# Performance work log

Hardware: AMD Instinct MI355X
Metric: run time of the kernel (lower is better)

Reference implementation:

```python
import jax, jax.numpy as jnp
import numpy as np

B, C, H, W = 16, 512, 16, 64
T = 128
V, E, EH, DH = 600, 80, 256, 512


def _lstm_scan(x_seq, h0, c0, Wih, Whh, b):
    # x_seq: [S, N, in]; PyTorch gate order i,f,g,o
    def step(carry, x):
        h, c = carry
        g = x @ Wih.T + h @ Whh.T + b
        i, f, gg, o = jnp.split(g, 4, axis=-1)
        c_new = jax.nn.sigmoid(f) * c + jax.nn.sigmoid(i) * jnp.tanh(gg)
        h_new = jax.nn.sigmoid(o) * jnp.tanh(c_new)
        return (h_new, c_new), h_new
    (hT, cT), hs = jax.lax.scan(step, (h0, c0), x_seq)
    return hs, hT, cT


def setup_inputs():
    key = jax.random.key(0)
    ks = jax.random.split(key, 32)
    INIT = 0.01
    def u(k, shape, s):
        return jax.random.uniform(k, shape, jnp.float32, -s, s)
    se = 1.0 / np.sqrt(EH)
    sd = 1.0 / np.sqrt(DH)
    sc = 1.0 / np.sqrt(DH + 2 * EH)
    so = 1.0 / np.sqrt(EH)
    sv = 1.0 / np.sqrt(2 * EH)
    return {
        'features': jax.random.normal(ks[0], (B, C, H, W), jnp.float32),
        'formulas': jax.random.randint(ks[1], (B, T), 0, V),
        'Wih_f': u(ks[2], (4 * EH, C), se), 'Whh_f': u(ks[3], (4 * EH, EH), se),
        'bih_f': u(ks[4], (4 * EH,), se), 'bhh_f': u(ks[5], (4 * EH,), se),
        'Wih_b': u(ks[6], (4 * EH, C), se), 'Whh_b': u(ks[7], (4 * EH, EH), se),
        'bih_b': u(ks[8], (4 * EH,), se), 'bhh_b': u(ks[9], (4 * EH,), se),
        'emb': jax.random.normal(ks[10], (V, E), jnp.float32),
        'Wc_w': u(ks[11], (EH, DH + 2 * EH), sc), 'Wc_b': u(ks[12], (EH,), sc),
        'Wout_w': u(ks[13], (V, EH), so), 'Wout_b': u(ks[14], (V,), so),
        'Vh0': u(ks[15], (2, EH), INIT), 'Vc0': u(ks[16], (2, EH), INIT),
        'beta': u(ks[17], (DH,), INIT),
        'Wh_w': u(ks[18], (DH, DH), sd), 'Wh_b': u(ks[19], (DH,), sd),
        'Wv_w': u(ks[20], (DH, 2 * EH), sv), 'Wv_b': u(ks[21], (DH,), sv),
        'Wdec_ih': u(ks[22], (4 * DH, EH + E), sd), 'Wdec_hh': u(ks[23], (4 * DH, DH), sd),
        'bdec_ih': u(ks[24], (4 * DH,), sd), 'bdec_hh': u(ks[25], (4 * DH,), sd),
    }


def _forward(features, formulas, Wih_f, Whh_f, bih_f, bhh_f, Wih_b, Whh_b, bih_b, bhh_b,
             emb, Wc_w, Wc_b, Wout_w, Wout_b, Vh0, Vc0, beta, Wh_w, Wh_b, Wv_w, Wv_b,
             Wdec_ih, Wdec_hh, bdec_ih, bdec_hh):
    Bv, Cv, Hv, Wd = features.shape
    eh = Vh0.shape[1]
    # ---- row encoder: bidirectional LSTM over width, batch = B*H ----
    x = features.transpose(0, 2, 3, 1).reshape(Bv * Hv, Wd, Cv).transpose(1, 0, 2)  # [W, B*H, C]
    h0f = jnp.broadcast_to(Vh0[0], (Bv * Hv, eh)); c0f = jnp.broadcast_to(Vc0[0], (Bv * Hv, eh))
    h0b = jnp.broadcast_to(Vh0[1], (Bv * Hv, eh)); c0b = jnp.broadcast_to(Vc0[1], (Bv * Hv, eh))
    hs_f, hTf, cTf = _lstm_scan(x, h0f, c0f, Wih_f, Whh_f, bih_f + bhh_f)
    hs_b, hTb, cTb = _lstm_scan(x[::-1], h0b, c0b, Wih_b, Whh_b, bih_b + bhh_b)
    hs_b = hs_b[::-1]
    enc_out = jnp.concatenate([hs_f, hs_b], -1).transpose(1, 0, 2).reshape(Bv, Hv, Wd, 2 * eh)

    def convert(s):  # [2, B*H, eh] -> [B, 2*eh]: permute, merge directions, mean over H
        return s.reshape(2, Bv, Hv, eh).transpose(1, 2, 0, 3).reshape(Bv, Hv, 2 * eh).mean(axis=1)
    h0 = convert(jnp.stack([hTf, hTb]))
    c0 = convert(jnp.stack([cTf, cTb]))
    ctx0 = enc_out.mean(axis=(1, 2))
    O0 = jnp.tanh(jnp.concatenate([h0, ctx0], 1) @ Wc_w.T + Wc_b)

    Wv_enc = enc_out @ Wv_w.T + Wv_b  # hoisted: W_v(enc_out) is constant across decode steps

    def dec_step(carry, tgt):
        h, c, O = carry
        prev_y = emb[tgt]                                   # [B, E]
        inp = jnp.concatenate([prev_y, O], 1)
        g = inp @ Wdec_ih.T + h @ Wdec_hh.T + bdec_ih + bdec_hh
        i, f, gg, o = jnp.split(g, 4, axis=-1)
        c_t = jax.nn.sigmoid(f) * c + jax.nn.sigmoid(i) * jnp.tanh(gg)
        h_t = jax.nn.sigmoid(o) * jnp.tanh(c_t)
        lin_h = h @ Wh_w.T + Wh_b                           # NB: attention uses PREVIOUS h, as in source
        e = jnp.sum(beta * jnp.tanh(lin_h[:, None, None, :] + Wv_enc), -1)  # [B, H, W]
        alpha = jax.nn.softmax(e.reshape(Bv, -1), -1).reshape(Bv, Hv, Wd)
        context = jnp.einsum('bhw,bhwd->bd', alpha, enc_out)
        O_t = jnp.tanh(jnp.concatenate([h_t, context], 1) @ Wc_w.T + Wc_b)
        logit = jax.nn.softmax(O_t @ Wout_w.T + Wout_b, -1)  # eval-mode softmax
        return (h_t, c_t, O_t), logit

    _, logits = jax.lax.scan(dec_step, (h0, c0, O0), formulas.T)
    return logits.transpose(1, 0, 2)  # [B, T, V]


def reference(features, formulas, Wih_f, Whh_f, bih_f, bhh_f, Wih_b, Whh_b, bih_b, bhh_b,
              emb, Wc_w, Wc_b, Wout_w, Wout_b, Vh0, Vc0, beta, Wh_w, Wh_b, Wv_w, Wv_b,
              Wdec_ih, Wdec_hh, bdec_ih, bdec_hh):
    logits = _forward(features, formulas, Wih_f, Whh_f, bih_f, bhh_f, Wih_b, Whh_b, bih_b, bhh_b,
                      emb, Wc_w, Wc_b, Wout_w, Wout_b, Vh0, Vc0, beta, Wh_w, Wh_b, Wv_w, Wv_b,
                      Wdec_ih, Wdec_hh, bdec_ih, bdec_hh)
    targets = jnp.argmax(logits, axis=2)  # argmax(log(p)) == argmax(p)
    return logits, targets
```

## Files before the change

### kernel.cpp

```cpp
#include <hip/hip_runtime.h>
#include <math.h>

#define NB 16
#define NC 512
#define NH 16
#define NW 64
#define NT 128
#define NV 600
#define NE 80
#define EH 256
#define DH 512
#define NSEQ 256
#define GEH 1024
#define GDH 2048

typedef float f32x4 __attribute__((ext_vector_type(4)));

#define OFF_XPRE_F 0ull
#define OFF_XPRE_B 16777216ull
#define OFF_XT     33554432ull
#define OFF_ENC    41943040ull
#define OFF_WENC   50331648ull
#define OFF_WDT    50855936ull
#define OFF_WHT    52592640ull
#define OFF_WCT    52854784ull
#define OFF_WOUTT  53116928ull
#define OFF_HA     53270528ull
#define OFF_CENC   53532672ull
#define OFF_CDEC   53663744ull
#define OFF_CTX0   53671936ull
#define OFF_OKT    53680128ull
#define WS_FLOATS  53708800ull

__device__ __forceinline__ float sigf(float x) {
  return __builtin_amdgcn_rcpf(1.f + __expf(-x));
}
__device__ __forceinline__ float tanhfast(float x) {
  float e = __expf(2.f * x);
  return 1.f - 2.f * __builtin_amdgcn_rcpf(e + 1.f);
}

__global__ void k_transpose(float* __restrict__ dst, const float* __restrict__ src,
                            int R, int Cc) {
  int idx = blockIdx.x * 256 + threadIdx.x;
  if (idx >= R * Cc) return;
  int c = idx / R, r = idx - c * R;
  dst[idx] = src[(size_t)r * Cc + c];
}

__global__ void k_prep_wenc(float* __restrict__ dst, const float* __restrict__ whh, int dir) {
  int idx = blockIdx.x * 256 + threadIdx.x;
  int g = idx & 3, j = (idx >> 2) & 255, k = idx >> 10;
  dst[(size_t)dir * 262144 + idx] = whh[((size_t)(g * 256 + j)) * 256 + k];
}

__global__ void k_buildXt(float* __restrict__ Xt, const float* __restrict__ feat) {
  __shared__ float tile[64][65];
  int n = blockIdx.x, cb = blockIdx.y * 64;
  int b = n >> 4, hh = n & 15;
  int tid = threadIdx.x;
  for (int i = 0; i < 16; ++i) {
    int c = (tid >> 6) + i * 4;
    int w = tid & 63;
    tile[c][w] = feat[(((size_t)b * NC + cb + c) * NH + hh) * NW + w];
  }
  __syncthreads();
  for (int i = 0; i < 16; ++i) {
    int w = (tid >> 6) + i * 4;
    int ci = tid & 63;
    Xt[((size_t)(w * NSEQ + n)) * NC + cb + ci] = tile[ci][w];
  }
}

__global__ __launch_bounds__(256) void k_gemm_nt(
    const float* __restrict__ A, const float* __restrict__ Wt,
    const float* __restrict__ bias1, const float* __restrict__ bias2,
    float* __restrict__ Cout, int M, int Nn, int K) {
  __shared__ float As[128 * 32];
  __shared__ float Bs[128 * 32];
  int tid = threadIdx.x;
  int mb = blockIdx.x * 128, nb = blockIdx.y * 128;
  int tx = tid & 15, ty = tid >> 4;
  int row0 = ty * 8, col0 = tx * 8;
  float acc[8][8];
#pragma unroll
  for (int i = 0; i < 8; ++i)
#pragma unroll
    for (int j = 0; j < 8; ++j) acc[i][j] = 0.f;
  int lm = tid >> 1, lk = (tid & 1) * 8;
  int sw = 4 * ((lm >> 3) & 7);
  int p0 = (lk + sw) & 31, p1 = (lk + 4 + sw) & 31;
  const float* Ap = A + (size_t)(mb + lm) * K + lk;
  const float* Bp = Wt + (size_t)(nb + lm) * K + lk;
  for (int k0 = 0; k0 < K; k0 += 16) {
    float4 a0 = *(const float4*)(Ap + k0);
    float4 a1 = *(const float4*)(Ap + k0 + 4);
    float4 b0 = *(const float4*)(Bp + k0);
    float4 b1 = *(const float4*)(Bp + k0 + 4);
    __syncthreads();
    *(float4*)&As[lm * 32 + p0] = a0;
    *(float4*)&As[lm * 32 + p1] = a1;
    *(float4*)&Bs[lm * 32 + p0] = b0;
    *(float4*)&Bs[lm * 32 + p1] = b1;
    __syncthreads();
#pragma unroll
    for (int kq = 0; kq < 4; ++kq) {
      float4 av[8], bv[8];
#pragma unroll
      for (int i = 0; i < 8; ++i) {
        int m = row0 + i;
        av[i] = *(float4*)&As[m * 32 + ((kq * 4 + 4 * ((m >> 3) & 7)) & 31)];
      }
#pragma unroll
      for (int j = 0; j < 8; ++j) {
        int n = col0 + j;
        bv[j] = *(float4*)&Bs[n * 32 + ((kq * 4 + 4 * ((n >> 3) & 7)) & 31)];
      }
#pragma unroll
      for (int i = 0; i < 8; ++i)
#pragma unroll
        for (int j = 0; j < 8; ++j)
          acc[i][j] += av[i].x * bv[j].x + av[i].y * bv[j].y
                     + av[i].z * bv[j].z + av[i].w * bv[j].w;
    }
  }
  float bs[8];
#pragma unroll
  for (int j = 0; j < 8; ++j) {
    float v = bias1 ? bias1[nb + col0 + j] : 0.f;
    if (bias2) v += bias2[nb + col0 + j];
    bs[j] = v;
  }
  for (int i = 0; i < 8; ++i) {
    float* cp = Cout + (size_t)(mb + row0 + i) * Nn + nb + col0;
#pragma unroll
    for (int j = 0; j < 8; ++j) cp[j] = acc[i][j] + bs[j];
  }
}

__global__ __launch_bounds__(1024) void k_encoder_s(
    const float* __restrict__ wenc, const float* __restrict__ xpreF,
    const float* __restrict__ xpreB, const float* __restrict__ Vh0,
    const float* __restrict__ Vc0, float* __restrict__ encout,
    float* __restrict__ hT_out, float* __restrict__ cT_out) {
  __shared__ float hs[4][256];
  __shared__ float pacc[3][16][256];
  int bid = blockIdx.x;
  int dir = bid >> 6;
  int s0 = (bid & 63) * 4;
  int tid = threadIdx.x;
  int j = tid & 255, kq = tid >> 8;
  float c[4];
  if (kq == 0) {
    float h0 = Vh0[dir * 256 + j];
    float c0v = Vc0[dir * 256 + j];
#pragma unroll
    for (int s = 0; s < 4; ++s) { hs[s][j] = h0; c[s] = c0v; }
  }
  __syncthreads();
  const float* wp = wenc + (size_t)dir * 262144 + (size_t)(kq * 64) * 1024 + (size_t)j * 4;
  const float* xbase = dir ? xpreB : xpreF;
  for (int t = 0; t < 64; ++t) {
    int w = dir ? (63 - t) : t;
    float acc[4][4];
#pragma unroll
    for (int s = 0; s < 4; ++s)
#pragma unroll
      for (int g = 0; g < 4; ++g) acc[s][g] = 0.f;
#pragma unroll 8
    for (int k = 0; k < 64; ++k) {
      float4 w4 = *(const float4*)(wp + (size_t)k * 1024);
      int kk = kq * 64 + k;
      float h0k = hs[0][kk], h1k = hs[1][kk], h2k = hs[2][kk], h3k = hs[3][kk];
      acc[0][0] += w4.x * h0k; acc[0][1] += w4.y * h0k; acc[0][2] += w4.z * h0k; acc[0][3] += w4.w * h0k;
      acc[1][0] += w4.x * h1k; acc[1][1] += w4.y * h1k; acc[1][2] += w4.z * h1k; acc[1][3] += w4.w * h1k;
      acc[2][0] += w4.x * h2k; acc[2][1] += w4.y * h2k; acc[2][2] += w4.z * h2k; acc[2][3] += w4.w * h2k;
      acc[3][0] += w4.x * h3k; acc[3][1] += w4.y * h3k; acc[3][2] += w4.z * h3k; acc[3][3] += w4.w * h3k;
    }
    if (kq > 0) {
#pragma unroll
      for (int s = 0; s < 4; ++s)
#pragma unroll
        for (int g = 0; g < 4; ++g)
          pacc[kq - 1][s * 4 + g][j] = acc[s][g];
    }
    __syncthreads();
    if (kq == 0) {
#pragma unroll
      for (int s = 0; s < 4; ++s) {
        int n = s0 + s;
        const float* xp = xbase + ((size_t)w * NSEQ + n) * GEH;
        float g4[4];
#pragma unroll
        for (int g = 0; g < 4; ++g)
          g4[g] = acc[s][g] + pacc[0][s * 4 + g][j] + pacc[1][s * 4 + g][j]
                + pacc[2][s * 4 + g][j] + xp[g * 256 + j];
        float cn = sigf(g4[1]) * c[s] + sigf(g4[0]) * tanhfast(g4[2]);
        c[s] = cn;
        float hn = sigf(g4[3]) * tanhfast(cn);
        hs[s][j] = hn;
        encout[((size_t)n * NW + w) * (2 * EH) + dir * EH + j] = hn;
      }
    }
    __syncthreads();
  }
  if (kq == 0) {
#pragma unroll
    for (int s = 0; s < 4; ++s) {
      int n = s0 + s;
      hT_out[((size_t)(dir * NSEQ + n)) * EH + j] = hs[s][j];
      cT_out[((size_t)(dir * NSEQ + n)) * EH + j] = c[s];
    }
  }
}

__global__ void k_conv(const float* __restrict__ hA, const float* __restrict__ cE,
                       const float* __restrict__ enc, float* __restrict__ cdec,
                       float* __restrict__ okT, float* __restrict__ ctx0) {
  int b = blockIdx.x, tid = threadIdx.x;
  for (int d = tid; d < 512; d += 256) {
    float s = 0.f;
    for (int p = 0; p < 1024; ++p) s += enc[((size_t)b * 1024 + p) * 512 + d];
    ctx0[(size_t)b * 512 + d] = s * (1.f / 1024.f);
    int dir = d >> 8, u = d & 255;
    float sh = 0.f, sc_ = 0.f;
    for (int hh = 0; hh < 16; ++hh) {
      size_t idx = ((size_t)(dir * NSEQ + b * 16 + hh)) * EH + u;
      sh += hA[idx]; sc_ += cE[idx];
    }
    cdec[(size_t)b * 512 + d] = sc_ * (1.f / 16.f);
    okT[(size_t)(256 + d) * 16 + b] = sh * (1.f / 16.f);
  }
}

__global__ void k_O0v2(const float* __restrict__ okT, const float* __restrict__ ctx0,
                       const float* __restrict__ wcT, const float* __restrict__ wcb,
                       const float* __restrict__ whT, const float* __restrict__ whb,
                       float* __restrict__ okT_o, float* __restrict__ linh) {
  int b = blockIdx.x, tid = threadIdx.x;
  float a = wcb[tid];
  for (int k = 0; k < 512; ++k)
    a += okT[(size_t)(256 + k) * 16 + b] * wcT[(size_t)k * 256 + tid];
  const float* cb = ctx0 + (size_t)b * 512;
  for (int k = 0; k < 512; ++k)
    a += cb[k] * wcT[(size_t)(512 + k) * 256 + tid];
  okT_o[(size_t)tid * 16 + b] = tanhfast(a);
  for (int d = tid; d < 512; d += 256) {
    float v = whb[d];
    for (int k = 0; k < 512; ++k)
      v += okT[(size_t)(256 + k) * 16 + b] * whT[(size_t)k * 512 + d];
    linh[(size_t)b * 512 + d] = v;
  }
}

__global__ void k_embproj(const int* __restrict__ formulas, const float* __restrict__ emb,
                          const float* __restrict__ wdT, const float* __restrict__ b1,
                          const float* __restrict__ b2, float* __restrict__ ep) {
  int g = blockIdx.x * 256 + threadIdx.x;
  int tb = blockIdx.y;
  int b = tb & 15, t = tb >> 4;
  int tok = formulas[b * NT + t];
  const float* ev = emb + (size_t)tok * NE;
  float a = b1[g] + b2[g];
  for (int k = 0; k < NE; ++k) a += ev[k] * wdT[(size_t)k * GDH + g];
  ep[(size_t)tb * GDH + g] = a;
}

__device__ __forceinline__ void logits_block(
    int vc, int lane, int wq, const float* __restrict__ okT,
    const float* __restrict__ woutT, const float* __restrict__ woutb,
    float* __restrict__ ev, float* __restrict__ evp) {
  int v = vc * 64 + lane;
  bool valid = v < NV;
  int vl = valid ? v : (NV - 1);
  float acc[4] = {0.f, 0.f, 0.f, 0.f};
  for (int k = 0; k < 256; ++k) {
    float w = woutT[(size_t)k * NV + vl];
    float4 o4 = *(const float4*)&okT[(size_t)k * 16 + wq * 4];
    acc[0] += w * o4.x; acc[1] += w * o4.y; acc[2] += w * o4.z; acc[3] += w * o4.w;
  }
  float bs = woutb[vl];
#pragma unroll
  for (int i = 0; i < 4; ++i) {
    float e = valid ? __expf(acc[i] + bs) : 0.f;
    if (valid) ev[(size_t)(wq * 4 + i) * NV + v] = e;
    float s = e;
#pragma unroll
    for (int m = 1; m < 64; m <<= 1) s += __shfl_xor(s, m, 64);
    if (lane == 0) evp[(wq * 4 + i) * 16 + vc] = s;
  }
}

__device__ __forceinline__ void norm_block(
    int b, int tid, const float* __restrict__ ev, const float* __restrict__ evp,
    float* __restrict__ outp, int t) {
  float tot = 0.f;
#pragma unroll
  for (int i = 0; i < 10; ++i) tot += evp[b * 16 + i];
  float r = __builtin_amdgcn_rcpf(tot);
  float* orow = outp + ((size_t)b * NT + t) * NV;
  orow[tid] = ev[b * NV + tid] * r;
  orow[tid + 256] = ev[b * NV + tid + 256] * r;
  if (tid < 88) orow[tid + 512] = ev[b * NV + tid + 512] * r;
}

__global__ __launch_bounds__(256) void k_dec1(
    const float* __restrict__ okT, const float* __restrict__ wdT,
    const float* __restrict__ woutT, const float* __restrict__ woutb,
    const float* __restrict__ linh, const float* __restrict__ beta,
    const float* __restrict__ wvenc, const float* __restrict__ enc,
    float* __restrict__ gpart, float* __restrict__ ctxp,
    float* __restrict__ spart, float* __restrict__ ev, float* __restrict__ evp,
    int t) {
  __shared__ float sscore[32];
  __shared__ float cpart[4][512];
  int bid = blockIdx.x, tid = threadIdx.x;
  int lane = tid & 63, wq = tid >> 6;

  if (bid < 512) {
    int b = bid >> 5, pc2 = bid & 31;
    int d0 = lane * 8;
    float lh[8], bt[8];
    const float* lp = linh + (size_t)b * 512 + d0;
#pragma unroll
    for (int jj = 0; jj < 8; ++jj) { lh[jj] = lp[jj]; bt[jj] = beta[d0 + jj]; }
    float c8[8] = {0.f, 0.f, 0.f, 0.f, 0.f, 0.f, 0.f, 0.f};
#pragma unroll
    for (int pi = 0; pi < 8; ++pi) {
      int p = pc2 * 32 + wq * 8 + pi;
      const float* wvp = wvenc + ((size_t)(b * 1024 + p)) * 512 + d0;
      const float* erp = enc + ((size_t)(b * 1024 + p)) * 512 + d0;
      f32x4 wv0 = __builtin_nontemporal_load((const f32x4*)wvp);
      f32x4 wv1 = __builtin_nontemporal_load((const f32x4*)(wvp + 4));
      f32x4 e0 = __builtin_nontemporal_load((const f32x4*)erp);
      f32x4 e1 = __builtin_nontemporal_load((const f32x4*)(erp + 4));
      float e = bt[0] * tanhfast(lh[0] + wv0.x) + bt[1] * tanhfast(lh[1] + wv0.y)
              + bt[2] * tanhfast(lh[2] + wv0.z) + bt[3] * tanhfast(lh[3] + wv0.w)
              + bt[4] * tanhfast(lh[4] + wv1.x) + bt[5] * tanhfast(lh[5] + wv1.y)
              + bt[6] * tanhfast(lh[6] + wv1.z) + bt[7] * tanhfast(lh[7] + wv1.w);
#pragma unroll
      for (int m = 1; m < 64; m <<= 1) e += __shfl_xor(e, m, 64);
      float s = __expf(e);
      if (lane == 0) sscore[wq * 8 + pi] = s;
      c8[0] += s * e0.x; c8[1] += s * e0.y; c8[2] += s * e0.z; c8[3] += s * e0.w;
      c8[4] += s * e1.x; c8[5] += s * e1.y; c8[6] += s * e1.z; c8[7] += s * e1.w;
    }
#pragma unroll
    for (int jj = 0; jj < 8; ++jj) cpart[wq][d0 + jj] = c8[jj];
    __syncthreads();
    {
      int d = tid * 2;
      float r0 = cpart[0][d] + cpart[1][d] + cpart[2][d] + cpart[3][d];
      float r1 = cpart[0][d + 1] + cpart[1][d + 1] + cpart[2][d + 1] + cpart[3][d + 1];
      *(float2*)&ctxp[((size_t)(b * 32 + pc2)) * 512 + d] = make_float2(r0, r1);
    }
    if (tid == 0) {
      float s = 0.f;
#pragma unroll
      for (int p = 0; p < 32; ++p) s += sscore[p];
      spart[b * 32 + pc2] = s;
    }
  } else if (bid < 560) {
    int idx = bid - 512;
    int oc = idx / 6, kc = idx - oc * 6;
    int o = oc * 256 + tid, k0 = kc * 128;
    const float* wp = wdT + (size_t)(80 + k0) * GDH + o;
    const float* sp = okT + (size_t)k0 * 16;
    float acc[16];
#pragma unroll
    for (int i = 0; i < 16; ++i) acc[i] = 0.f;
    for (int kk = 0; kk < 128; ++kk) {
      float w = wp[(size_t)kk * GDH];
#pragma unroll
      for (int bb = 0; bb < 16; ++bb) acc[bb] += sp[kk * 16 + bb] * w;
    }
#pragma unroll
    for (int bb = 0; bb < 16; ++bb)
      gpart[((size_t)(kc * 16 + bb)) * GDH + o] = acc[bb];
  } else {
    if (t > 0) logits_block(bid - 560, lane, wq, okT, woutT, woutb, ev, evp);
  }
}

__global__ __launch_bounds__(256) void k_dec2(
    const float* __restrict__ gpart, const float* __restrict__ ep,
    const float* __restrict__ ctxp, const float* __restrict__ spart,
    const float* __restrict__ wcT, const float* __restrict__ wcb,
    const float* __restrict__ whT, const float* __restrict__ whb,
    const float* __restrict__ ev, const float* __restrict__ evp,
    float* __restrict__ cdecA, float* __restrict__ cdecB,
    float* __restrict__ okT, float* __restrict__ linh,
    float* __restrict__ outp, int t) {
  __shared__ float smem[1280];
  int bid = blockIdx.x, tid = threadIdx.x;
  if (bid < 64) {
    int b = bid >> 2, q = bid & 3;
    const float* cold = (t & 1) ? cdecB : cdecA;
    float* cnew = (t & 1) ? cdecA : cdecB;
    float Ssum = 0.f;
#pragma unroll
    for (int pc = 0; pc < 32; ++pc) Ssum += spart[b * 32 + pc];
    float rS = __builtin_amdgcn_rcpf(Ssum);
    {
      int d = tid * 2;
      float s0 = 0.f, s1 = 0.f;
#pragma unroll 4
      for (int pc = 0; pc < 32; ++pc) {
        float2 c2 = *(const float2*)&ctxp[((size_t)(b * 32 + pc)) * 512 + d];
        s0 += c2.x; s1 += c2.y;
      }
      smem[512 + d] = s0 * rS;
      smem[512 + d + 1] = s1 * rS;
    }
#pragma unroll
    for (int half = 0; half < 2; ++half) {
      int j = half * 256 + tid;
      float g4[4];
#pragma unroll
      for (int gi = 0; gi < 4; ++gi) {
        float v = ep[((size_t)(t * 16 + b)) * GDH + gi * 512 + j];
#pragma unroll
        for (int kc = 0; kc < 6; ++kc)
          v += gpart[((size_t)(kc * 16 + b)) * GDH + gi * 512 + j];
        g4[gi] = v;
      }
      size_t ci = (size_t)b * 512 + j;
      float cn = sigf(g4[1]) * cold[ci] + sigf(g4[0]) * tanhfast(g4[2]);
      cnew[ci] = cn;
      float hn = sigf(g4[3]) * tanhfast(cn);
      smem[j] = hn;
      okT[(size_t)(256 + j) * 16 + b] = hn;
    }
    __syncthreads();
    {
      int ol = tid & 63, kq = tid >> 6;
      int o = q * 64 + ol;
      float a = 0.f;
      const float* wp = wcT + (size_t)(kq * 256) * 256 + o;
      const float* sp = smem + kq * 256;
      for (int k = 0; k < 256; ++k) a += wp[(size_t)k * 256] * sp[k];
      smem[1024 + kq * 64 + ol] = a;
    }
    __syncthreads();
    if (tid < 64) {
      float s = smem[1024 + tid] + smem[1088 + tid] + smem[1152 + tid] + smem[1216 + tid];
      int o = q * 64 + tid;
      okT[(size_t)o * 16 + b] = tanhfast(s + wcb[o]);
    }
    __syncthreads();
    {
      int o2 = tid & 127, kh = tid >> 7;
      int o = q * 128 + o2;
      float a = 0.f;
      const float* wp = whT + (size_t)(kh * 256) * 512 + o;
      const float* sp = smem + kh * 256;
      for (int k = 0; k < 256; ++k) a += wp[(size_t)k * 512] * sp[k];
      smem[1024 + kh * 128 + o2] = a;
    }
    __syncthreads();
    if (tid < 128) {
      int o = q * 128 + tid;
      float s = smem[1024 + tid] + smem[1152 + tid];
      linh[(size_t)b * 512 + o] = s + whb[o];
    }
  } else {
    if (t > 0) norm_block(bid - 64, tid, ev, evp, outp, t - 1);
  }
}

__global__ __launch_bounds__(256) void k_log_tail(
    const float* __restrict__ okT, const float* __restrict__ woutT,
    const float* __restrict__ woutb, float* __restrict__ ev, float* __restrict__ evp) {
  int lane = threadIdx.x & 63, wq = threadIdx.x >> 6;
  logits_block(blockIdx.x, lane, wq, okT, woutT, woutb, ev, evp);
}

__global__ void k_norm(const float* __restrict__ ev, const float* __restrict__ evp,
                       float* __restrict__ outp, int t) {
  norm_block(blockIdx.x, threadIdx.x, ev, evp, outp, t);
}

__global__ void k_argmax(const float* __restrict__ outp, float* __restrict__ tgt) {
  int bt = blockIdx.x;
  int lane = threadIdx.x;
  const float* row = outp + (size_t)bt * NV;
  float bv = -1.f;
  int bi = 0;
  for (int v = lane; v < NV; v += 64) {
    float x = row[v];
    if (x > bv) { bv = x; bi = v; }
  }
#pragma unroll
  for (int m = 1; m < 64; m <<= 1) {
    float ov = __shfl_xor(bv, m, 64);
    int oi = __shfl_xor(bi, m, 64);
    if (ov > bv || (ov == bv && oi < bi)) { bv = ov; bi = oi; }
  }
  if (lane == 0) tgt[bt] = (float)bi;
}

extern "C" void kernel_launch(void* const* d_in, const int* in_sizes, int n_in,
                              void* d_out, int out_size, void* d_ws, size_t ws_size,
                              hipStream_t stream) {
  (void)in_sizes; (void)n_in; (void)out_size;
  if (ws_size < WS_FLOATS * sizeof(float)) return;

  const float* feat     = (const float*)d_in[0];
  const int*   formulas = (const int*)d_in[1];
  const float* Wih_f    = (const float*)d_in[2];
  const float* Whh_f    = (const float*)d_in[3];
  const float* bih_f    = (const float*)d_in[4];
  const float* bhh_f    = (const float*)d_in[5];
  const float* Wih_b    = (const float*)d_in[6];
  const float* Whh_b    = (const float*)d_in[7];
  const float* bih_b    = (const float*)d_in[8];
  const float* bhh_b    = (const float*)d_in[9];
  const float* emb      = (const float*)d_in[10];
  const float* Wc_w     = (const float*)d_in[11];
  const float* Wc_b     = (const float*)d_in[12];
  const float* Wout_w   = (const float*)d_in[13];
  const float* Wout_b   = (const float*)d_in[14];
  const float* Vh0      = (const float*)d_in[15];
  const float* Vc0      = (const float*)d_in[16];
  const float* beta     = (const float*)d_in[17];
  const float* Wh_w     = (const float*)d_in[18];
  const float* Wh_b     = (const float*)d_in[19];
  const float* Wv_w     = (const float*)d_in[20];
  const float* Wv_b     = (const float*)d_in[21];
  const float* Wdec_ih  = (const float*)d_in[22];
  const float* Wdec_hh  = (const float*)d_in[23];
  const float* bdec_ih  = (const float*)d_in[24];
  const float* bdec_hh  = (const float*)d_in[25];

  float* ws = (float*)d_ws;
  float* xpreF  = ws + OFF_XPRE_F;
  float* xpreB  = ws + OFF_XPRE_B;
  float* xt     = ws + OFF_XT;
  float* encout = ws + OFF_ENC;
  float* wenc   = ws + OFF_WENC;
  float* wdT    = ws + OFF_WDT;
  float* whT    = ws + OFF_WHT;
  float* wcT    = ws + OFF_WCT;
  float* woutT  = ws + OFF_WOUTT;
  float* hA     = ws + OFF_HA;
  float* cenc   = ws + OFF_CENC;
  float* cdecA  = ws + OFF_CDEC;
  float* ctx0   = ws + OFF_CTX0;
  float* okT    = ws + OFF_OKT;
  float* gpart  = xpreB;
  float* ctxp   = gpart + 196608;
  float* spart  = ctxp + 262144;
  float* ev     = spart + 512;
  float* evp    = ev + 9600;
  float* linh   = evp + 256;
  float* cdecB  = linh + 8192;
  float* embproj = xpreF;
  float* wvenc   = xt;

  float* out_logits = (float*)d_out;
  float* out_tgt    = out_logits + (size_t)NB * NT * NV;

  k_transpose<<<(2048 * 336 + 255) / 256, 256, 0, stream>>>(wdT, Wdec_ih, 2048, 336);
  k_transpose<<<(2048 * 512 + 255) / 256, 256, 0, stream>>>(wdT + 336 * 2048, Wdec_hh, 2048, 512);
  k_transpose<<<(512 * 512 + 255) / 256, 256, 0, stream>>>(whT, Wh_w, 512, 512);
  k_transpose<<<(256 * 1024 + 255) / 256, 256, 0, stream>>>(wcT, Wc_w, 256, 1024);
  k_transpose<<<(600 * 256 + 255) / 256, 256, 0, stream>>>(woutT, Wout_w, 600, 256);
  k_prep_wenc<<<1024, 256, 0, stream>>>(wenc, Whh_f, 0);
  k_prep_wenc<<<1024, 256, 0, stream>>>(wenc, Whh_b, 1);
  k_buildXt<<<dim3(256, 8), 256, 0, stream>>>(xt, feat);
  k_gemm_nt<<<dim3(128, 8), 256, 0, stream>>>(xt, Wih_f, bih_f, bhh_f, xpreF, 16384, 1024, 512);
  k_gemm_nt<<<dim3(128, 8), 256, 0, stream>>>(xt, Wih_b, bih_b, bhh_b, xpreB, 16384, 1024, 512);

  k_encoder_s<<<128, 1024, 0, stream>>>(wenc, xpreF, xpreB, Vh0, Vc0, encout, hA, cenc);

  k_gemm_nt<<<dim3(128, 4), 256, 0, stream>>>(encout, Wv_w, Wv_b, nullptr, wvenc, 16384, 512, 512);
  k_conv<<<16, 256, 0, stream>>>(hA, cenc, encout, cdecA, okT, ctx0);
  k_O0v2<<<16, 256, 0, stream>>>(okT, ctx0, wcT, Wc_b, whT, Wh_b, okT, linh);
  k_embproj<<<dim3(8, 2048), 256, 0, stream>>>(formulas, emb, wdT, bdec_ih, bdec_hh, embproj);

  for (int t = 0; t < NT; ++t) {
    k_dec1<<<570, 256, 0, stream>>>(okT, wdT, woutT, Wout_b, linh, beta, wvenc, encout,
                                    gpart, ctxp, spart, ev, evp, t);
    k_dec2<<<80, 256, 0, stream>>>(gpart, embproj, ctxp, spart, wcT, Wc_b, whT, Wh_b,
                                   ev, evp, cdecA, cdecB, okT, linh, out_logits, t);
  }
  k_log_tail<<<10, 256, 0, stream>>>(okT, woutT, Wout_b, ev, evp);
  k_norm<<<16, 256, 0, stream>>>(ev, evp, out_logits, NT - 1);
  k_argmax<<<NB * NT, 64, 0, stream>>>(out_logits, out_tgt);
}
```

Baseline: 7.547 ms.

## Split decoder attention over more blocks and tile embedding projection over tokens

```diff
diff --git a/kernel.cpp b/kernel.cpp
--- a/kernel.cpp
+++ b/kernel.cpp
@@ -253,17 +253,34 @@
   }
 }
 
-__global__ void k_embproj(const int* __restrict__ formulas, const float* __restrict__ emb,
-                          const float* __restrict__ wdT, const float* __restrict__ b1,
-                          const float* __restrict__ b2, float* __restrict__ ep) {
-  int g = blockIdx.x * 256 + threadIdx.x;
-  int tb = blockIdx.y;
-  int b = tb & 15, t = tb >> 4;
-  int tok = formulas[b * NT + t];
-  const float* ev = emb + (size_t)tok * NE;
-  float a = b1[g] + b2[g];
-  for (int k = 0; k < NE; ++k) a += ev[k] * wdT[(size_t)k * GDH + g];
-  ep[(size_t)tb * GDH + g] = a;
+__global__ __launch_bounds__(256) void k_embproj(
+    const int* __restrict__ formulas, const float* __restrict__ emb,
+    const float* __restrict__ wdT, const float* __restrict__ b1,
+    const float* __restrict__ b2, float* __restrict__ ep) {
+  __shared__ float se[32][NE];
+  int gc = blockIdx.x, tc = blockIdx.y;
+  int tid = threadIdx.x;
+  int g = gc * 256 + tid;
+  for (int i = tid; i < 32 * NE; i += 256) {
+    int ti = i / NE, k = i - ti * NE;
+    int tb = tc * 32 + ti;
+    int b = tb & 15, t = tb >> 4;
+    int tok = formulas[b * NT + t];
+    se[ti][k] = emb[(size_t)tok * NE + k];
+  }
+  __syncthreads();
+  float acc[32];
+  float bias = b1[g] + b2[g];
+#pragma unroll
+  for (int i = 0; i < 32; ++i) acc[i] = bias;
+  for (int k = 0; k < NE; ++k) {
+    float w = wdT[(size_t)k * GDH + g];
+#pragma unroll
+    for (int i = 0; i < 32; ++i) acc[i] += se[i][k] * w;
+  }
+#pragma unroll
+  for (int i = 0; i < 32; ++i)
+    ep[(size_t)(tc * 32 + i) * GDH + g] = acc[i];
 }
 
 __device__ __forceinline__ void logits_block(
@@ -312,13 +329,13 @@
     float* __restrict__ gpart, float* __restrict__ ctxp,
     float* __restrict__ spart, float* __restrict__ ev, float* __restrict__ evp,
     int t) {
-  __shared__ float sscore[32];
+  __shared__ float sscore[16];
   __shared__ float cpart[4][512];
   int bid = blockIdx.x, tid = threadIdx.x;
   int lane = tid & 63, wq = tid >> 6;
 
-  if (bid < 512) {
-    int b = bid >> 5, pc2 = bid & 31;
+  if (bid < 1024) {
+    int b = bid >> 6, pc = bid & 63;
     int d0 = lane * 8;
     float lh[8], bt[8];
     const float* lp = linh + (size_t)b * 512 + d0;
@@ -326,8 +343,8 @@
     for (int jj = 0; jj < 8; ++jj) { lh[jj] = lp[jj]; bt[jj] = beta[d0 + jj]; }
     float c8[8] = {0.f, 0.f, 0.f, 0.f, 0.f, 0.f, 0.f, 0.f};
 #pragma unroll
-    for (int pi = 0; pi < 8; ++pi) {
-      int p = pc2 * 32 + wq * 8 + pi;
+    for (int pi = 0; pi < 4; ++pi) {
+      int p = pc * 16 + wq * 4 + pi;
       const float* wvp = wvenc + ((size_t)(b * 1024 + p)) * 512 + d0;
       const float* erp = enc + ((size_t)(b * 1024 + p)) * 512 + d0;
       f32x4 wv0 = __builtin_nontemporal_load((const f32x4*)wvp);
@@ -341,7 +358,7 @@
 #pragma unroll
       for (int m = 1; m < 64; m <<= 1) e += __shfl_xor(e, m, 64);
       float s = __expf(e);
-      if (lane == 0) sscore[wq * 8 + pi] = s;
+      if (lane == 0) sscore[wq * 4 + pi] = s;
       c8[0] += s * e0.x; c8[1] += s * e0.y; c8[2] += s * e0.z; c8[3] += s * e0.w;
       c8[4] += s * e1.x; c8[5] += s * e1.y; c8[6] += s * e1.z; c8[7] += s * e1.w;
     }
@@ -352,16 +369,16 @@
       int d = tid * 2;
       float r0 = cpart[0][d] + cpart[1][d] + cpart[2][d] + cpart[3][d];
       float r1 = cpart[0][d + 1] + cpart[1][d + 1] + cpart[2][d + 1] + cpart[3][d + 1];
-      *(float2*)&ctxp[((size_t)(b * 32 + pc2)) * 512 + d] = make_float2(r0, r1);
+      *(float2*)&ctxp[((size_t)(b * 64 + pc)) * 512 + d] = make_float2(r0, r1);
     }
     if (tid == 0) {
       float s = 0.f;
 #pragma unroll
-      for (int p = 0; p < 32; ++p) s += sscore[p];
-      spart[b * 32 + pc2] = s;
-    }
-  } else if (bid < 560) {
-    int idx = bid - 512;
+      for (int p = 0; p < 16; ++p) s += sscore[p];
+      spart[b * 64 + pc] = s;
+    }
+  } else if (bid < 1072) {
+    int idx = bid - 1024;
     int oc = idx / 6, kc = idx - oc * 6;
     int o = oc * 256 + tid, k0 = kc * 128;
     const float* wp = wdT + (size_t)(80 + k0) * GDH + o;
@@ -378,7 +395,7 @@
     for (int bb = 0; bb < 16; ++bb)
       gpart[((size_t)(kc * 16 + bb)) * GDH + o] = acc[bb];
   } else {
-    if (t > 0) logits_block(bid - 560, lane, wq, okT, woutT, woutb, ev, evp);
+    if (t > 0) logits_block(bid - 1072, lane, wq, okT, woutT, woutb, ev, evp);
   }
 }
 
@@ -399,14 +416,14 @@
     float* cnew = (t & 1) ? cdecA : cdecB;
     float Ssum = 0.f;
 #pragma unroll
-    for (int pc = 0; pc < 32; ++pc) Ssum += spart[b * 32 + pc];
+    for (int pc = 0; pc < 64; ++pc) Ssum += spart[b * 64 + pc];
     float rS = __builtin_amdgcn_rcpf(Ssum);
     {
       int d = tid * 2;
       float s0 = 0.f, s1 = 0.f;
-#pragma unroll 4
-      for (int pc = 0; pc < 32; ++pc) {
-        float2 c2 = *(const float2*)&ctxp[((size_t)(b * 32 + pc)) * 512 + d];
+#pragma unroll 8
+      for (int pc = 0; pc < 64; ++pc) {
+        float2 c2 = *(const float2*)&ctxp[((size_t)(b * 64 + pc)) * 512 + d];
         s0 += c2.x; s1 += c2.y;
       }
       smem[512 + d] = s0 * rS;
@@ -549,8 +566,8 @@
   float* okT    = ws + OFF_OKT;
   float* gpart  = xpreB;
   float* ctxp   = gpart + 196608;
-  float* spart  = ctxp + 262144;
-  float* ev     = spart + 512;
+  float* spart  = ctxp + 524288;
+  float* ev     = spart + 1024;
   float* evp    = ev + 9600;
   float* linh   = evp + 256;
   float* cdecB  = linh + 8192;
@@ -576,11 +593,11 @@
   k_gemm_nt<<<dim3(128, 4), 256, 0, stream>>>(encout, Wv_w, Wv_b, nullptr, wvenc, 16384, 512, 512);
   k_conv<<<16, 256, 0, stream>>>(hA, cenc, encout, cdecA, okT, ctx0);
   k_O0v2<<<16, 256, 0, stream>>>(okT, ctx0, wcT, Wc_b, whT, Wh_b, okT, linh);
-  k_embproj<<<dim3(8, 2048), 256, 0, stream>>>(formulas, emb, wdT, bdec_ih, bdec_hh, embproj);
+  k_embproj<<<dim3(8, 64), 256, 0, stream>>>(formulas, emb, wdT, bdec_ih, bdec_hh, embproj);
 
   for (int t = 0; t < NT; ++t) {
-    k_dec1<<<570, 256, 0, stream>>>(okT, wdT, woutT, Wout_b, linh, beta, wvenc, encout,
-                                    gpart, ctxp, spart, ev, evp, t);
+    k_dec1<<<1082, 256, 0, stream>>>(okT, wdT, woutT, Wout_b, linh, beta, wvenc, encout,
+                                     gpart, ctxp, spart, ev, evp, t);
     k_dec2<<<80, 256, 0, stream>>>(gpart, embproj, ctxp, spart, wcT, Wc_b, whT, Wh_b,
                                    ev, evp, cdecA, cdecB, okT, linh, out_logits, t);
   }
```

Result: slower. 7.986 ms (+5.8%).
